# Optimization experiments

Measured on AMD Instinct MI355X. Metric: run time of the kernel, lower is better.

## Reference

```python
import jax, jax.numpy as jnp
import numpy as np

N_NODES = 50000
N_EDGES = 800000
DIM = 256
HEADS = 8
DIM_OUT = 32  # per-head; dim_inner = HEADS*DIM_OUT = 256


def setup_inputs() -> dict:
    key = jax.random.key(0)
    ks = jax.random.split(key, 9)
    s = 1.0 / np.sqrt(DIM)
    inner = HEADS * DIM_OUT
    return {
        "x": jax.random.normal(ks[0], (N_NODES, DIM), dtype=jnp.float32),
        "Wq": jax.random.uniform(ks[1], (DIM, inner), jnp.float32, -s, s),
        "bq": jax.random.uniform(ks[2], (inner,), jnp.float32, -s, s),
        "Wk": jax.random.uniform(ks[3], (DIM, inner), jnp.float32, -s, s),
        "bk": jax.random.uniform(ks[4], (inner,), jnp.float32, -s, s),
        "Wv": jax.random.uniform(ks[5], (DIM, inner), jnp.float32, -s, s),
        "bv": jax.random.uniform(ks[6], (inner,), jnp.float32, -s, s),
        "src": jax.random.randint(ks[7], (N_EDGES,), 0, N_NODES),
        "dst": jax.random.randint(ks[8], (N_EDGES,), 0, N_NODES),
    }


def reference(x, Wq, bq, Wk, bk, Wv, bv, src, dst):
    n = x.shape[0]
    q = (x @ Wq + bq).reshape(n, HEADS, DIM_OUT)
    k = (x @ Wk + bk).reshape(n, HEADS, DIM_OUT)
    v = (x @ Wv + bv).reshape(n, HEADS, DIM_OUT)
    # edge-wise u_dot_v: dot of src query with dst key, per head -> [E, H]
    scores = jnp.einsum('ehd,ehd->eh', q[src], k[dst]) / jnp.sqrt(
        jnp.asarray(DIM_OUT, dtype=x.dtype))
    # segment softmax over incoming edges of each destination node
    m = jax.ops.segment_max(scores, dst, num_segments=n)  # [N, H]
    m = jnp.where(jnp.isfinite(m), m, 0.0)
    e = jnp.exp(scores - m[dst])
    z = jax.ops.segment_sum(e, dst, num_segments=n)  # [N, H]
    p = e / jnp.maximum(z[dst], 1e-16)  # [E, H]
    # u_mul_e_sum: sum over incoming edges of src values weighted by attn
    out = jax.ops.segment_sum(v[src] * p[:, :, None], dst, num_segments=n)
    return out.reshape(n, HEADS * DIM_OUT)  # concat=True
```

## Files before the change

kernel.cpp:

```cpp
#include <hip/hip_runtime.h>
#include <math.h>

#define N_NODES 50000
#define N_EDGES 800000
#define DIM 256
#define HEADS 8
#define DIM_OUT 32
#define INNER 256
#define M_PAD 50048

typedef __attribute__((ext_vector_type(8))) short bf16x8;
typedef __attribute__((ext_vector_type(4))) float f32x4;
typedef __attribute__((ext_vector_type(2))) float f32x2;

__device__ __forceinline__ unsigned short f2bf(float f) {
    unsigned u = __float_as_uint(f);
    unsigned r = (u + 0x7FFFu + ((u >> 16) & 1u)) >> 16;
    return (unsigned short)r;
}

__device__ __forceinline__ f32x2 up2(unsigned u) {
    f32x2 r;
    r.x = __uint_as_float(u << 16);
    r.y = __uint_as_float(u & 0xFFFF0000u);
    return r;
}
__device__ __forceinline__ void up2x4(uint4 r, f32x2* o) {
    o[0] = up2(r.x); o[1] = up2(r.y); o[2] = up2(r.z); o[3] = up2(r.w);
}

__device__ __forceinline__ void gll16(const void* g, void* l) {
    __builtin_amdgcn_global_load_lds(
        (const __attribute__((address_space(1))) unsigned*)(uintptr_t)g,
        (__attribute__((address_space(3))) unsigned*)(unsigned)(uintptr_t)l,
        16, 0, 0);
}

#define NB_CONVX 6256
#define NB_CONVW 768
#define NB_HIST  3125
__global__ __launch_bounds__(256) void prep(
    const float* __restrict__ x,
    const float* __restrict__ Wq, const float* __restrict__ Wk,
    const float* __restrict__ Wv,
    const int* __restrict__ dst,
    unsigned short* __restrict__ xbf, unsigned short* __restrict__ Wt,
    int* __restrict__ deg)
{
    int b = blockIdx.x;
    if (b < NB_CONVX) {
        size_t i8 = ((size_t)b * 256 + threadIdx.x) * 8;
        unsigned short h[8];
        if (i8 < (size_t)N_NODES * 256) {
            float4 a = *(const float4*)(x + i8);
            float4 c = *(const float4*)(x + i8 + 4);
            h[0]=f2bf(a.x); h[1]=f2bf(a.y); h[2]=f2bf(a.z); h[3]=f2bf(a.w);
            h[4]=f2bf(c.x); h[5]=f2bf(c.y); h[6]=f2bf(c.z); h[7]=f2bf(c.w);
        } else {
            #pragma unroll
            for (int j = 0; j < 8; j++) h[j] = 0;
        }
        uint4 o;
        o.x = (unsigned)h[0] | ((unsigned)h[1] << 16);
        o.y = (unsigned)h[2] | ((unsigned)h[3] << 16);
        o.z = (unsigned)h[4] | ((unsigned)h[5] << 16);
        o.w = (unsigned)h[6] | ((unsigned)h[7] << 16);
        *(uint4*)(xbf + i8) = o;
    } else if (b < NB_CONVX + NB_CONVW) {
        int idx = (b - NB_CONVX) * 256 + threadIdx.x;
        int z = idx >> 16, r = idx & 65535;
        int k = r >> 8, n = r & 255;
        const float* W = (z == 0) ? Wq : (z == 1) ? Wk : Wv;
        Wt[(size_t)z * 65536 + n * 256 + k] = f2bf(W[k * 256 + n]);
    } else {
        int e = (b - NB_CONVX - NB_CONVW) * 256 + threadIdx.x;
        if (e < N_EDGES) atomicAdd(deg + dst[e], 1);
    }
}

#define GEMM_NWG 2346
__global__ __launch_bounds__(256) void gemm_qkv(
    const unsigned short* __restrict__ xbf,
    const unsigned short* __restrict__ Wt,
    const float* __restrict__ bq, const float* __restrict__ bk,
    const float* __restrict__ bv,
    unsigned short* __restrict__ q, unsigned short* __restrict__ k,
    unsigned short* __restrict__ v)
{
    int hw = blockIdx.x;
    int xcd = hw & 7, pos = hw >> 3;
    const int q8 = GEMM_NWG >> 3, r8 = GEMM_NWG & 7;
    int lid = (xcd < r8 ? xcd * (q8 + 1) : r8 * (q8 + 1) + (xcd - r8) * q8) + pos;
    int xx = lid / 6;
    int yz = lid - xx * 6;
    const int row0 = xx * 128;
    const int col0 = (yz & 1) * 128;
    const int z = yz >> 1;

    const int t = threadIdx.x;
    const unsigned short* Wz = Wt + (size_t)z * 65536;
    const float* bias = (z == 0) ? bq : (z == 1) ? bk : bv;
    unsigned short* C = (z == 0) ? q : (z == 1) ? k : v;

    __shared__ __align__(16) short As[128 * 32];
    __shared__ __align__(16) short Bs[128 * 32];

    const int wave = t >> 6;
    const int lane = t & 63;
    const int wm = (wave & 1) * 64;
    const int wn = (wave >> 1) * 64;
    const int lr = lane & 15;
    const int lg = lane >> 4;
    const int srow = lane >> 2;
    const int sch  = lane & 3;

    f32x4 acc[4][4] = {};

    for (int k0 = 0; k0 < 256; k0 += 32) {
        #pragma unroll
        for (int c = 0; c < 2; c++) {
            int seg = wave * 2 + c;
            gll16(xbf + (size_t)(row0 + seg * 16 + srow) * 256 + k0 + sch * 8,
                  As + seg * 512);
        }
        #pragma unroll
        for (int c = 0; c < 2; c++) {
            int seg = wave * 2 + c;
            gll16(Wz + (size_t)(col0 + seg * 16 + srow) * 256 + k0 + sch * 8,
                  Bs + seg * 512);
        }
        __syncthreads();

        bf16x8 af[4], bfr[4];
        #pragma unroll
        for (int mi = 0; mi < 4; mi++)
            af[mi] = *(const bf16x8*)&As[(wm + mi * 16 + lr) * 32 + lg * 8];
        #pragma unroll
        for (int ni = 0; ni < 4; ni++)
            bfr[ni] = *(const bf16x8*)&Bs[(wn + ni * 16 + lr) * 32 + lg * 8];
        #pragma unroll
        for (int mi = 0; mi < 4; mi++)
            #pragma unroll
            for (int ni = 0; ni < 4; ni++)
                acc[mi][ni] = __builtin_amdgcn_mfma_f32_16x16x32_bf16(
                    af[mi], bfr[ni], acc[mi][ni], 0, 0, 0);
        __syncthreads();
    }

    #pragma unroll
    for (int mi = 0; mi < 4; mi++) {
        #pragma unroll
        for (int ni = 0; ni < 4; ni++) {
            int gcol = col0 + wn + ni * 16 + lr;
            float bb = bias[gcol];
            #pragma unroll
            for (int r = 0; r < 4; r++) {
                int grow = row0 + wm + mi * 16 + lg * 4 + r;
                if (grow < N_NODES)
                    C[(size_t)grow * 256 + gcol] = f2bf(acc[mi][ni][r] + bb);
            }
        }
    }
}

__global__ __launch_bounds__(1024) void scan_deg(
    const int* __restrict__ deg, int* __restrict__ rowptr)
{
    __shared__ int wsum[16];
    __shared__ int wpre[16];
    int t = threadIdx.x;
    int wid = t >> 6, ln = t & 63;
    int carry = 0;
    for (int base = 0; base < N_NODES; base += 4096) {
        int i4 = base + t * 4;
        int4 dv = {0, 0, 0, 0};
        if (i4 < N_NODES) dv = *(const int4*)(deg + i4);
        int sum = dv.x + dv.y + dv.z + dv.w;
        int inc = sum;
        #pragma unroll
        for (int off = 1; off < 64; off <<= 1) {
            int u = __shfl_up(inc, off);
            if (ln >= off) inc += u;
        }
        if (ln == 63) wsum[wid] = inc;
        __syncthreads();
        if (wid == 0 && ln < 16) {
            int s = wsum[ln];
            int p = s;
            #pragma unroll
            for (int off = 1; off < 16; off <<= 1) {
                int u = __shfl_up(p, off);
                if (ln >= off) p += u;
            }
            wpre[ln] = p - s;
        }
        __syncthreads();
        if (i4 < N_NODES) {
            int r = carry + wpre[wid] + (inc - sum);
            r += dv.x; rowptr[i4 + 1] = r;
            r += dv.y; rowptr[i4 + 2] = r;
            r += dv.z; rowptr[i4 + 3] = r;
            r += dv.w; rowptr[i4 + 4] = r;
        }
        carry += wpre[15] + wsum[15];
        __syncthreads();
    }
    if (t == 0) rowptr[0] = 0;
}

__global__ __launch_bounds__(256) void csr_scatter(
    const int* __restrict__ src, const int* __restrict__ dst,
    const int* __restrict__ rowptr,
    int* __restrict__ deg, int* __restrict__ edge_src)
{
    int e = blockIdx.x * 256 + threadIdx.x;
    if (e >= N_EDGES) return;
    int d = dst[e];
    int old = atomicSub(deg + d, 1);
    edge_src[rowptr[d] + old - 1] = src[e];
}

__global__ __launch_bounds__(256) void node_attn(
    const unsigned short* __restrict__ qbf,
    const unsigned short* __restrict__ kbf,
    const unsigned short* __restrict__ vbf,
    const int* __restrict__ rowptr, const int* __restrict__ edge_src,
    float* __restrict__ out)
{
    int node = blockIdx.x * 4 + (threadIdx.x >> 6);
    int lane = threadIdx.x & 63;
    if (node >= N_NODES) return;
    const int half = lane >> 5;
    const int l = lane & 31;

    int beg = rowptr[node], end = rowptr[node + 1];
    int deg = end - beg;

    float* op = out + (size_t)node * 256 + l * 8;
    if (deg <= 0) {
        if (half == 0) {
            float4 z4 = {0.f, 0.f, 0.f, 0.f};
            *(float4*)op = z4;
            *(float4*)(op + 4) = z4;
        }
        return;
    }

    f32x2 kf2[4];
    up2x4(*(const uint4*)(kbf + (size_t)node * 256 + l * 8), kf2);

    const unsigned short* qrow = qbf + l * 8;
    const unsigned short* vrow = vbf + l * 8;

    const float SC = 0.17677669529663687f * 1.4426950408889634f;

    int U = (deg + 1) >> 1;
    U = ((U + 2) / 3) * 3;
    U = __builtin_amdgcn_readfirstlane(U);

    const int i0 = beg + half;
    const int last = end - 1;

    int tmp0 = edge_src[min(i0,     last)];
    int tmp1 = edge_src[min(i0 + 2, last)];
    int idC  = edge_src[min(i0 + 4, last)];
    int idA  = edge_src[min(i0 + 6, last)];
    int idB  = 0;
    uint4 qA = *(const uint4*)(qrow + (size_t)tmp0 * 256);
    uint4 vA = *(const uint4*)(vrow + (size_t)tmp0 * 256);
    uint4 qB = *(const uint4*)(qrow + (size_t)tmp1 * 256);
    uint4 vB = *(const uint4*)(vrow + (size_t)tmp1 * 256);
    uint4 qC, vC;

    float m = -1e30f, zsum = 0.0f;
    f32x2 af2[4] = {};

#define BODY(QW, VW, QL, VL, IDL, IDF, P)                                    \
    do {                                                                     \
        size_t off_ = (size_t)(IDL) * 256;                                   \
        QL = *(const uint4*)(qrow + off_);                                   \
        VL = *(const uint4*)(vrow + off_);                                   \
        int vi_ = i0 + 2 * t + 2 * (P);                                      \
        IDF = edge_src[min(vi_ + 8, last)];                                  \
        f32x2 qf_[4], vf_[4];                                                \
        up2x4(QW, qf_);                                                      \
        up2x4(VW, vf_);                                                      \
        f32x2 d_ = qf_[0] * kf2[0];                                          \
        d_ += qf_[1] * kf2[1];                                               \
        d_ += qf_[2] * kf2[2];                                               \
        d_ += qf_[3] * kf2[3];                                               \
        float s_ = d_.x + d_.y;                                              \
        s_ += __shfl_xor(s_, 1);                                             \
        s_ += __shfl_xor(s_, 2);                                             \
        bool ok_ = vi_ < end;                                                \
        float sc_ = ok_ ? s_ * SC : -1e30f;                                  \
        float mn_ = fmaxf(m, sc_);                                           \
        float w_ = exp2f(sc_ - mn_);                                         \
        w_ = ok_ ? w_ : 0.0f;                                                \
        float al_ = exp2f(m - mn_);                                          \
        zsum = zsum * al_ + w_;                                              \
        f32x2 a2_ = {al_, al_}, w2_ = {w_, w_};                              \
        af2[0] = af2[0] * a2_ + vf_[0] * w2_;                                \
        af2[1] = af2[1] * a2_ + vf_[1] * w2_;                                \
        af2[2] = af2[2] * a2_ + vf_[2] * w2_;                                \
        af2[3] = af2[3] * a2_ + vf_[3] * w2_;                                \
        m = mn_;                                                             \
    } while (0)

    for (int t = 0; t < U; t += 3) {
        BODY(qA, vA, qC, vC, idC, idB, 0);
        BODY(qB, vB, qA, vA, idA, idC, 1);
        BODY(qC, vC, qB, vB, idB, idA, 2);
    }
#undef BODY

    float mo = __shfl_xor(m, 32);
    float mt = fmaxf(m, mo);
    float scale = exp2f(m - mt);
    zsum *= scale;
    zsum += __shfl_xor(zsum, 32);
    #pragma unroll
    for (int j = 0; j < 4; j++) {
        af2[j].x = af2[j].x * scale;
        af2[j].y = af2[j].y * scale;
        af2[j].x += __shfl_xor(af2[j].x, 32);
        af2[j].y += __shfl_xor(af2[j].y, 32);
    }

    float inv = 1.0f / fmaxf(zsum, 1e-16f);
    if (half == 0) {
        float4 o0 = {af2[0].x * inv, af2[0].y * inv, af2[1].x * inv, af2[1].y * inv};
        float4 o1 = {af2[2].x * inv, af2[2].y * inv, af2[3].x * inv, af2[3].y * inv};
        *(float4*)op = o0;
        *(float4*)(op + 4) = o1;
    }
}

extern "C" void kernel_launch(void* const* d_in, const int* in_sizes, int n_in,
                              void* d_out, int out_size, void* d_ws, size_t ws_size,
                              hipStream_t stream) {
    const float* x  = (const float*)d_in[0];
    const float* Wq = (const float*)d_in[1];
    const float* bq = (const float*)d_in[2];
    const float* Wk = (const float*)d_in[3];
    const float* bk = (const float*)d_in[4];
    const float* Wv = (const float*)d_in[5];
    const float* bv = (const float*)d_in[6];
    const int* src  = (const int*)d_in[7];
    const int* dst  = (const int*)d_in[8];
    float* out = (float*)d_out;

    unsigned short* qbf = (unsigned short*)d_ws;
    unsigned short* kbf = qbf + (size_t)N_NODES * INNER;
    unsigned short* vbf = kbf + (size_t)N_NODES * INNER;
    unsigned short* xbf = vbf + (size_t)N_NODES * INNER;
    unsigned short* Wt  = xbf + (size_t)M_PAD * INNER;
    int* deg      = (int*)(Wt + 3 * 65536);
    int* rowptr   = deg + N_NODES;
    int* edge_src = rowptr + (N_NODES + 1);

    hipMemsetAsync(deg, 0, (size_t)N_NODES * sizeof(int), stream);

    prep<<<NB_CONVX + NB_CONVW + NB_HIST, 256, 0, stream>>>(
        x, Wq, Wk, Wv, dst, xbf, Wt, deg);

    gemm_qkv<<<GEMM_NWG, 256, 0, stream>>>(xbf, Wt, bq, bk, bv, qbf, kbf, vbf);

    scan_deg<<<1, 1024, 0, stream>>>(deg, rowptr);
    csr_scatter<<<(N_EDGES + 255) / 256, 256, 0, stream>>>(
        src, dst, rowptr, deg, edge_src);

    node_attn<<<(N_NODES + 3) / 4, 256, 0, stream>>>(
        qbf, kbf, vbf, rowptr, edge_src, out);
}
```

Baseline: 366.6 us.

## Fold degree scan into GEMM launch, widen GEMM K-tile, deepen attention prefetch

The separate single-block scan kernel is removed and its work runs as an extra block of the QKV GEMM launch, so the scan overlaps with the GEMM and one launch is saved. The GEMM K-step grows from 32 to 64, halving the number of barrier pairs at the cost of twice the shared memory. The node attention loop goes from a 3-stage to a 4-stage rotating prefetch of gathered q/v rows with deeper edge-index lookahead, and gets a launch-bounds occupancy hint. The deeper pipeline raises register pressure, and the scan block, now using 256 threads, may finish after the GEMM blocks.

```diff
diff --git a/kernel.cpp b/kernel.cpp
--- a/kernel.cpp
+++ b/kernel.cpp
@@ -85,8 +85,50 @@
     const float* __restrict__ bq, const float* __restrict__ bk,
     const float* __restrict__ bv,
     unsigned short* __restrict__ q, unsigned short* __restrict__ k,
-    unsigned short* __restrict__ v)
+    unsigned short* __restrict__ v,
+    const int* __restrict__ deg, int* __restrict__ rowptr)
 {
+    const int t = threadIdx.x;
+
+    if (blockIdx.x == GEMM_NWG) {
+        __shared__ int wsum4[4];
+        __shared__ int wpre4[5];
+        int wid = t >> 6, ln = t & 63;
+        int carry = 0;
+        for (int base = 0; base < N_NODES; base += 1024) {
+            int i4 = base + t * 4;
+            int4 dv = {0, 0, 0, 0};
+            if (i4 < N_NODES) dv = *(const int4*)(deg + i4);
+            int sum = dv.x + dv.y + dv.z + dv.w;
+            int inc = sum;
+            #pragma unroll
+            for (int off = 1; off < 64; off <<= 1) {
+                int u = __shfl_up(inc, off);
+                if (ln >= off) inc += u;
+            }
+            if (ln == 63) wsum4[wid] = inc;
+            __syncthreads();
+            if (t == 0) {
+                int a = 0;
+                #pragma unroll
+                for (int j = 0; j < 4; j++) { wpre4[j] = a; a += wsum4[j]; }
+                wpre4[4] = a;
+            }
+            __syncthreads();
+            if (i4 < N_NODES) {
+                int r = carry + wpre4[wid] + (inc - sum);
+                r += dv.x; rowptr[i4 + 1] = r;
+                r += dv.y; rowptr[i4 + 2] = r;
+                r += dv.z; rowptr[i4 + 3] = r;
+                r += dv.w; rowptr[i4 + 4] = r;
+            }
+            carry += wpre4[4];
+            __syncthreads();
+        }
+        if (t == 0) rowptr[0] = 0;
+        return;
+    }
+
     int hw = blockIdx.x;
     int xcd = hw & 7, pos = hw >> 3;
     const int q8 = GEMM_NWG >> 3, r8 = GEMM_NWG & 7;
@@ -97,13 +139,12 @@
     const int col0 = (yz & 1) * 128;
     const int z = yz >> 1;
 
-    const int t = threadIdx.x;
     const unsigned short* Wz = Wt + (size_t)z * 65536;
     const float* bias = (z == 0) ? bq : (z == 1) ? bk : bv;
     unsigned short* C = (z == 0) ? q : (z == 1) ? k : v;
 
-    __shared__ __align__(16) short As[128 * 32];
-    __shared__ __align__(16) short Bs[128 * 32];
+    __shared__ __align__(16) short As[128 * 64];
+    __shared__ __align__(16) short Bs[128 * 64];
 
     const int wave = t >> 6;
     const int lane = t & 63;
@@ -111,39 +152,42 @@
     const int wn = (wave >> 1) * 64;
     const int lr = lane & 15;
     const int lg = lane >> 4;
-    const int srow = lane >> 2;
-    const int sch  = lane & 3;
+    const int srow = lane >> 3;
+    const int sch  = lane & 7;
 
     f32x4 acc[4][4] = {};
 
-    for (int k0 = 0; k0 < 256; k0 += 32) {
+    for (int k0 = 0; k0 < 256; k0 += 64) {
         #pragma unroll
-        for (int c = 0; c < 2; c++) {
-            int seg = wave * 2 + c;
-            gll16(xbf + (size_t)(row0 + seg * 16 + srow) * 256 + k0 + sch * 8,
+        for (int c = 0; c < 4; c++) {
+            int seg = wave * 4 + c;
+            gll16(xbf + (size_t)(row0 + seg * 8 + srow) * 256 + k0 + sch * 8,
                   As + seg * 512);
         }
         #pragma unroll
-        for (int c = 0; c < 2; c++) {
-            int seg = wave * 2 + c;
-            gll16(Wz + (size_t)(col0 + seg * 16 + srow) * 256 + k0 + sch * 8,
+        for (int c = 0; c < 4; c++) {
+            int seg = wave * 4 + c;
+            gll16(Wz + (size_t)(col0 + seg * 8 + srow) * 256 + k0 + sch * 8,
                   Bs + seg * 512);
         }
         __syncthreads();
 
-        bf16x8 af[4], bfr[4];
         #pragma unroll
-        for (int mi = 0; mi < 4; mi++)
-            af[mi] = *(const bf16x8*)&As[(wm + mi * 16 + lr) * 32 + lg * 8];
-        #pragma unroll
-        for (int ni = 0; ni < 4; ni++)
-            bfr[ni] = *(const bf16x8*)&Bs[(wn + ni * 16 + lr) * 32 + lg * 8];
-        #pragma unroll
-        for (int mi = 0; mi < 4; mi++)
+        for (int kk = 0; kk < 64; kk += 32) {
+            bf16x8 af[4], bfr[4];
+            #pragma unroll
+            for (int mi = 0; mi < 4; mi++)
+                af[mi] = *(const bf16x8*)&As[(wm + mi * 16 + lr) * 64 + kk + lg * 8];
             #pragma unroll
             for (int ni = 0; ni < 4; ni++)
-                acc[mi][ni] = __builtin_amdgcn_mfma_f32_16x16x32_bf16(
-                    af[mi], bfr[ni], acc[mi][ni], 0, 0, 0);
+                bfr[ni] = *(const bf16x8*)&Bs[(wn + ni * 16 + lr) * 64 + kk + lg * 8];
+            #pragma unroll
+            for (int mi = 0; mi < 4; mi++)
+                #pragma unroll
+                for (int ni = 0; ni < 4; ni++)
+                    acc[mi][ni] = __builtin_amdgcn_mfma_f32_16x16x32_bf16(
+                        af[mi], bfr[ni], acc[mi][ni], 0, 0, 0);
+        }
         __syncthreads();
     }
 
@@ -161,51 +205,6 @@
             }
         }
     }
-}
-
-__global__ __launch_bounds__(1024) void scan_deg(
-    const int* __restrict__ deg, int* __restrict__ rowptr)
-{
-    __shared__ int wsum[16];
-    __shared__ int wpre[16];
-    int t = threadIdx.x;
-    int wid = t >> 6, ln = t & 63;
-    int carry = 0;
-    for (int base = 0; base < N_NODES; base += 4096) {
-        int i4 = base + t * 4;
-        int4 dv = {0, 0, 0, 0};
-        if (i4 < N_NODES) dv = *(const int4*)(deg + i4);
-        int sum = dv.x + dv.y + dv.z + dv.w;
-        int inc = sum;
-        #pragma unroll
-        for (int off = 1; off < 64; off <<= 1) {
-            int u = __shfl_up(inc, off);
-            if (ln >= off) inc += u;
-        }
-        if (ln == 63) wsum[wid] = inc;
-        __syncthreads();
-        if (wid == 0 && ln < 16) {
-            int s = wsum[ln];
-            int p = s;
-            #pragma unroll
-            for (int off = 1; off < 16; off <<= 1) {
-                int u = __shfl_up(p, off);
-                if (ln >= off) p += u;
-            }
-            wpre[ln] = p - s;
-        }
-        __syncthreads();
-        if (i4 < N_NODES) {
-            int r = carry + wpre[wid] + (inc - sum);
-            r += dv.x; rowptr[i4 + 1] = r;
-            r += dv.y; rowptr[i4 + 2] = r;
-            r += dv.z; rowptr[i4 + 3] = r;
-            r += dv.w; rowptr[i4 + 4] = r;
-        }
-        carry += wpre[15] + wsum[15];
-        __syncthreads();
-    }
-    if (t == 0) rowptr[0] = 0;
 }
 
 __global__ __launch_bounds__(256) void csr_scatter(
@@ -220,7 +219,7 @@
     edge_src[rowptr[d] + old - 1] = src[e];
 }
 
-__global__ __launch_bounds__(256) void node_attn(
+__global__ __launch_bounds__(256, 7) void node_attn(
     const unsigned short* __restrict__ qbf,
     const unsigned short* __restrict__ kbf,
     const unsigned short* __restrict__ vbf,
@@ -255,33 +254,37 @@
     const float SC = 0.17677669529663687f * 1.4426950408889634f;
 
     int U = (deg + 1) >> 1;
-    U = ((U + 2) / 3) * 3;
+    U = ((U + 3) >> 2) << 2;
     U = __builtin_amdgcn_readfirstlane(U);
 
     const int i0 = beg + half;
     const int last = end - 1;
 
-    int tmp0 = edge_src[min(i0,     last)];
-    int tmp1 = edge_src[min(i0 + 2, last)];
-    int idC  = edge_src[min(i0 + 4, last)];
-    int idA  = edge_src[min(i0 + 6, last)];
-    int idB  = 0;
-    uint4 qA = *(const uint4*)(qrow + (size_t)tmp0 * 256);
-    uint4 vA = *(const uint4*)(vrow + (size_t)tmp0 * 256);
-    uint4 qB = *(const uint4*)(qrow + (size_t)tmp1 * 256);
-    uint4 vB = *(const uint4*)(vrow + (size_t)tmp1 * 256);
-    uint4 qC, vC;
+    int t0  = edge_src[min(i0,      last)];
+    int t1  = edge_src[min(i0 + 2,  last)];
+    int t2  = edge_src[min(i0 + 4,  last)];
+    int id3 = edge_src[min(i0 + 6,  last)];
+    int id4 = edge_src[min(i0 + 8,  last)];
+    int id5 = edge_src[min(i0 + 10, last)];
+    int id6 = edge_src[min(i0 + 12, last)];
+    uint4 qA = *(const uint4*)(qrow + (size_t)t0 * 256);
+    uint4 vA = *(const uint4*)(vrow + (size_t)t0 * 256);
+    uint4 qB = *(const uint4*)(qrow + (size_t)t1 * 256);
+    uint4 vB = *(const uint4*)(vrow + (size_t)t1 * 256);
+    uint4 qC = *(const uint4*)(qrow + (size_t)t2 * 256);
+    uint4 vC = *(const uint4*)(vrow + (size_t)t2 * 256);
+    uint4 qD = {}, vD = {};
 
     float m = -1e30f, zsum = 0.0f;
     f32x2 af2[4] = {};
 
-#define BODY(QW, VW, QL, VL, IDL, IDF, P)                                    \
+#define BODY(QW, VW, QL, VL, IDR, P)                                         \
     do {                                                                     \
-        size_t off_ = (size_t)(IDL) * 256;                                   \
+        size_t off_ = (size_t)(IDR) * 256;                                   \
         QL = *(const uint4*)(qrow + off_);                                   \
         VL = *(const uint4*)(vrow + off_);                                   \
-        int vi_ = i0 + 2 * t + 2 * (P);                                      \
-        IDF = edge_src[min(vi_ + 8, last)];                                  \
+        int vi_ = i0 + 2 * (t + (P));                                        \
+        IDR = edge_src[min(vi_ + 14, last)];                                 \
         f32x2 qf_[4], vf_[4];                                                \
         up2x4(QW, qf_);                                                      \
         up2x4(VW, vf_);                                                      \
@@ -307,10 +310,11 @@
         m = mn_;                                                             \
     } while (0)
 
-    for (int t = 0; t < U; t += 3) {
-        BODY(qA, vA, qC, vC, idC, idB, 0);
-        BODY(qB, vB, qA, vA, idA, idC, 1);
-        BODY(qC, vC, qB, vB, idB, idA, 2);
+    for (int t = 0; t < U; t += 4) {
+        BODY(qA, vA, qD, vD, id3, 0);
+        BODY(qB, vB, qA, vA, id4, 1);
+        BODY(qC, vC, qB, vB, id5, 2);
+        BODY(qD, vD, qC, vC, id6, 3);
     }
 #undef BODY
 
@@ -364,9 +368,9 @@
     prep<<<NB_CONVX + NB_CONVW + NB_HIST, 256, 0, stream>>>(
         x, Wq, Wk, Wv, dst, xbf, Wt, deg);
 
-    gemm_qkv<<<GEMM_NWG, 256, 0, stream>>>(xbf, Wt, bq, bk, bv, qbf, kbf, vbf);
-
-    scan_deg<<<1, 1024, 0, stream>>>(deg, rowptr);
+    gemm_qkv<<<GEMM_NWG + 1, 256, 0, stream>>>(
+        xbf, Wt, bq, bk, bv, qbf, kbf, vbf, deg, rowptr);
+
     csr_scatter<<<(N_EDGES + 255) / 256, 256, 0, stream>>>(
         src, dst, rowptr, deg, edge_src);
 
```

Result: slower. 484.7 us (+32.2%).
